# Optimization experiments

Hardware: AMD Instinct MI355X
Metric: run time of the kernel (lower is better)

## Reference

```python
import jax, jax.numpy as jnp
import numpy as np

N_USERS = 100000
N_MOVIES = 100000
N_EDGES = 1000000
HIDDEN = 128


def setup_inputs() -> dict:
    key = jax.random.key(0)
    k1, k2, k3, k4, k5, k6, k7 = jax.random.split(key, 7)
    user_features = jax.random.normal(k1, (N_USERS, HIDDEN), dtype=jnp.float32)
    movie_features = jax.random.normal(k2, (N_MOVIES, HIDDEN), dtype=jnp.float32)
    src = jax.random.randint(k3, (N_EDGES,), 0, N_USERS, dtype=jnp.int64 if jax.config.jax_enable_x64 else jnp.int32)
    dst = jax.random.randint(k4, (N_EDGES,), 0, N_MOVIES, dtype=jnp.int64 if jax.config.jax_enable_x64 else jnp.int32)
    edge_index = jnp.stack([src, dst], axis=0)
    # Linear(2*HIDDEN, HIDDEN) params, torch-style init (kaiming uniform ~ U(-1/sqrt(fan_in), 1/sqrt(fan_in)))
    b1_bound = 1.0 / np.sqrt(2 * HIDDEN)
    W1 = jax.random.uniform(k5, (2 * HIDDEN, HIDDEN), minval=-b1_bound, maxval=b1_bound, dtype=jnp.float32)
    b1 = jax.random.uniform(k6, (HIDDEN,), minval=-b1_bound, maxval=b1_bound, dtype=jnp.float32)
    b2_bound = 1.0 / np.sqrt(HIDDEN)
    k8, k9 = jax.random.split(k7)
    W2 = jax.random.uniform(k8, (HIDDEN, 1), minval=-b2_bound, maxval=b2_bound, dtype=jnp.float32)
    b2 = jax.random.uniform(k9, (1,), minval=-b2_bound, maxval=b2_bound, dtype=jnp.float32)
    return {"user_features": user_features, "movie_features": movie_features,
            "edge_index": edge_index, "W1": W1, "b1": b1, "W2": W2, "b2": b2}


def reference(user_features, movie_features, edge_index, W1, b1, W2, b2):
    # Gather endpoint features per edge: [E, H] each
    u = user_features[edge_index[0]]
    m = movie_features[edge_index[1]]
    edge_feats = jnp.concatenate([u, m], axis=1)  # [E, 2H]
    h = jax.nn.relu(edge_feats @ W1 + b1)         # [E, H]
    out = h @ W2 + b2                             # [E, 1]
    return out.reshape(-1)
```

## Files before the change

### kernel.cpp

```cpp
#include <hip/hip_runtime.h>
#include <hip/hip_bf16.h>

typedef short s8v __attribute__((ext_vector_type(8)));
typedef float f4v __attribute__((ext_vector_type(4)));

__device__ __forceinline__ unsigned int bfround(float f) {
    unsigned int x = __float_as_uint(f);
    return (x + 0x7fffu + ((x >> 16) & 1u)) >> 16;
}
__device__ __forceinline__ unsigned int pkbf(float x, float y) {
    __hip_bfloat162 h = __float22bfloat162_rn(make_float2(x, y));
    return *(unsigned int*)&h;
}
__device__ __forceinline__ float i8f(unsigned int w, int k) {
    return (float)((int)(signed char)(w >> (8 * k)));
}

__global__ __launch_bounds__(256) void pack_w(const float* __restrict__ W1,
                                              uint4* __restrict__ WF)
{
    const int half = blockIdx.x;
    #pragma unroll
    for (int iter = 0; iter < 8; ++iter) {
        int idx  = iter * 256 + threadIdx.x;
        int lane = idx & 63;
        int t    = (idx >> 6) & 7;
        int c    = idx >> 9;
        int q = lane >> 4, m = lane & 15;
        unsigned int w[4];
        #pragma unroll
        for (int jj = 0; jj < 4; ++jj) {
            float lo = W1[(size_t)(half * 128 + c * 32 + q * 8 + 2 * jj    ) * 128 + t * 16 + m];
            float hi = W1[(size_t)(half * 128 + c * 32 + q * 8 + 2 * jj + 1) * 128 + t * 16 + m];
            w[jj] = bfround(lo) | (bfround(hi) << 16);
        }
        WF[(size_t)half * 2048 + idx] = make_uint4(w[0], w[1], w[2], w[3]);
    }
}

__global__ __launch_bounds__(256, 2) void proj_kernel(
    const float* __restrict__ userf, const float* __restrict__ movief,
    const uint4* __restrict__ WF, const float* __restrict__ b1,
    uint2* __restrict__ Pu, uint2* __restrict__ Pm,
    float* __restrict__ SU, float* __restrict__ SM,
    int ntiles, int bph)
{
    const int half = blockIdx.x >= bph;
    const int bid  = half ? blockIdx.x - bph : blockIdx.x;
    const float* __restrict__ feat = half ? movief : userf;
    uint2* __restrict__ P = half ? Pm : Pu;
    float* __restrict__ S = half ? SM : SU;
    const uint4* __restrict__ wfh = WF + (size_t)half * 2048;

    const int lane = threadIdx.x & 63;
    const int m    = lane & 15;
    const int q    = lane >> 4;

    s8v bfrag[8][4];
    #pragma unroll
    for (int c = 0; c < 4; ++c)
        #pragma unroll
        for (int t = 0; t < 8; ++t) {
            uint4 f = wfh[(c * 8 + t) * 64 + lane];
            bfrag[t][c] = *(const s8v*)&f;
        }

    float bias_v[8];
    #pragma unroll
    for (int t = 0; t < 8; ++t)
        bias_v[t] = half ? b1[t * 16 + m] : 0.0f;

    const int wid = bid * 4 + (threadIdx.x >> 6);
    const int nw  = bph * 4;

#define LOAD_A(dst, t_) do {                                            \
        const float4* arow_ = (const float4*)feat + (size_t)(t_) * 512; \
        _Pragma("unroll")                                               \
        for (int c_ = 0; c_ < 4; ++c_) {                                \
            dst[c_][0] = arow_[m * 32 + c_ * 8 + q * 2 + 0];            \
            dst[c_][1] = arow_[m * 32 + c_ * 8 + q * 2 + 1];            \
        }                                                               \
    } while (0)

    float4 a[4][2];
    int tile = wid;
    if (tile < ntiles) LOAD_A(a, tile);

    while (tile < ntiles) {
        const int nxt = tile + nw;
        float4 an[4][2];
        if (nxt < ntiles) LOAD_A(an, nxt);

        f4v acc[8];
        #pragma unroll
        for (int t = 0; t < 8; ++t)
            acc[t] = (f4v){bias_v[t], bias_v[t], bias_v[t], bias_v[t]};

        #pragma unroll
        for (int c = 0; c < 4; ++c) {
            uint4 aw;
            aw.x = pkbf(a[c][0].x, a[c][0].y);
            aw.y = pkbf(a[c][0].z, a[c][0].w);
            aw.z = pkbf(a[c][1].x, a[c][1].y);
            aw.w = pkbf(a[c][1].z, a[c][1].w);
            s8v af = *(const s8v*)&aw;

            #pragma unroll
            for (int t = 0; t < 8; ++t)
                acc[t] = __builtin_amdgcn_mfma_f32_16x16x32_bf16(af, bfrag[t][c], acc[t], 0, 0, 0);
        }

        #pragma unroll
        for (int r = 0; r < 4; ++r) {
            float mx = 0.0f;
            #pragma unroll
            for (int t = 0; t < 8; ++t) mx = fmaxf(mx, fabsf(acc[t][r]));
            #pragma unroll
            for (int off = 1; off < 16; off <<= 1)
                mx = fmaxf(mx, __shfl_xor(mx, off, 64));
            float inv = mx > 0.0f ? 127.0f / mx : 0.0f;

            unsigned int lo = 0, hi = 0;
            #pragma unroll
            for (int t = 0; t < 4; ++t) {
                lo |= ((unsigned int)(__float2int_rn(acc[t][r]     * inv) & 0xff)) << (8 * t);
                hi |= ((unsigned int)(__float2int_rn(acc[t + 4][r] * inv) & 0xff)) << (8 * t);
            }
            int row = tile * 16 + q * 4 + r;
            P[(size_t)row * 16 + m] = make_uint2(lo, hi);
            if (m == 0) S[row] = mx * (1.0f / 127.0f);
        }

        #pragma unroll
        for (int c = 0; c < 4; ++c) {
            a[c][0] = an[c][0];
            a[c][1] = an[c][1];
        }
        tile = nxt;
    }
#undef LOAD_A
}

__global__ __launch_bounds__(256) void edge_kernel(
    const int* __restrict__ src, const int* __restrict__ dst,
    const uint2* __restrict__ Pu, const uint2* __restrict__ Pm,
    const float* __restrict__ SU, const float* __restrict__ SM,
    const float* __restrict__ W2, const float* __restrict__ b2,
    float* __restrict__ out)
{
    const int lane = threadIdx.x & 63;
    const int L    = lane & 15;
    const int g    = lane >> 4;
    const int eg   = (blockIdx.x * 4 + (threadIdx.x >> 6)) * 16 + g * 4;

    float w2v[8];
    #pragma unroll
    for (int j = 0; j < 8; ++j) w2v[j] = W2[j * 16 + L];

    int si[4], di[4];
    #pragma unroll
    for (int i = 0; i < 4; ++i) { si[i] = src[eg + i]; di[i] = dst[eg + i]; }

    uint2 pu[4], pm[4];
    float scu[4], scm[4];
    #pragma unroll
    for (int i = 0; i < 4; ++i) {
        pu[i] = Pu[(size_t)si[i] * 16 + L];
        pm[i] = Pm[(size_t)di[i] * 16 + L];
        scu[i] = SU[si[i]];
        scm[i] = SM[di[i]];
    }

    float res[4];
    #pragma unroll
    for (int i = 0; i < 4; ++i) {
        const unsigned int uw[2] = {pu[i].x, pu[i].y};
        const unsigned int mw[2] = {pm[i].x, pm[i].y};
        float acc = 0.0f;
        #pragma unroll
        for (int v = 0; v < 2; ++v) {
            #pragma unroll
            for (int k = 0; k < 4; ++k) {
                float h = fmaf(scu[i], i8f(uw[v], k), scm[i] * i8f(mw[v], k));
                acc = fmaf(fmaxf(h, 0.0f), w2v[v * 4 + k], acc);
            }
        }
        #pragma unroll
        for (int off = 1; off < 16; off <<= 1)
            acc += __shfl_xor(acc, off, 64);
        res[i] = acc;
    }

    if (L == 0) {
        float bb = b2[0];
        *(float4*)(out + eg) = make_float4(res[0] + bb, res[1] + bb, res[2] + bb, res[3] + bb);
    }
}

extern "C" void kernel_launch(void* const* d_in, const int* in_sizes, int n_in,
                              void* d_out, int out_size, void* d_ws, size_t ws_size,
                              hipStream_t stream) {
    const float* userf  = (const float*)d_in[0];
    const float* movief = (const float*)d_in[1];
    const int*   eidx   = (const int*)d_in[2];
    const float* W1     = (const float*)d_in[3];
    const float* b1     = (const float*)d_in[4];
    const float* W2     = (const float*)d_in[5];
    const float* b2     = (const float*)d_in[6];
    float* out = (float*)d_out;

    const int NU = in_sizes[0] / 128;
    const int NM = in_sizes[1] / 128;
    const int E  = in_sizes[2] / 2;

    uint2* Pu = (uint2*)d_ws;
    uint2* Pm = Pu + (size_t)NU * 16;
    float* SU = (float*)(Pm + (size_t)NM * 16);
    float* SM = SU + NU;
    uint4* WF = (uint4*)(SM + NM);

    const int ntiles = NU / 16;
    const int bph    = 512;

    pack_w<<<2, 256, 0, stream>>>(W1, WF);
    proj_kernel<<<2 * bph, 256, 0, stream>>>(userf, movief, WF, b1, Pu, Pm, SU, SM, ntiles, bph);
    edge_kernel<<<E / 64, 256, 0, stream>>>(eidx, eidx + E, Pu, Pm, SU, SM, W2, b2, out);
}
```

Baseline: 184.9 us.

## Deepen proj_kernel prefetch to two tiles and coalesce scale stores

```diff
diff --git a/kernel.cpp b/kernel.cpp
--- a/kernel.cpp
+++ b/kernel.cpp
@@ -82,14 +82,14 @@
         }                                                               \
     } while (0)
 
-    float4 a[4][2];
+    float4 a0[4][2], a1[4][2], a2[4][2];
     int tile = wid;
-    if (tile < ntiles) LOAD_A(a, tile);
+    if (tile < ntiles)          LOAD_A(a0, tile);
+    if (tile + nw < ntiles)     LOAD_A(a1, tile + nw);
 
     while (tile < ntiles) {
-        const int nxt = tile + nw;
-        float4 an[4][2];
-        if (nxt < ntiles) LOAD_A(an, nxt);
+        const int pf = tile + 2 * nw;
+        if (pf < ntiles) LOAD_A(a2, pf);
 
         f4v acc[8];
         #pragma unroll
@@ -99,10 +99,10 @@
         #pragma unroll
         for (int c = 0; c < 4; ++c) {
             uint4 aw;
-            aw.x = pkbf(a[c][0].x, a[c][0].y);
-            aw.y = pkbf(a[c][0].z, a[c][0].w);
-            aw.z = pkbf(a[c][1].x, a[c][1].y);
-            aw.w = pkbf(a[c][1].z, a[c][1].w);
+            aw.x = pkbf(a0[c][0].x, a0[c][0].y);
+            aw.y = pkbf(a0[c][0].z, a0[c][0].w);
+            aw.z = pkbf(a0[c][1].x, a0[c][1].y);
+            aw.w = pkbf(a0[c][1].z, a0[c][1].w);
             s8v af = *(const s8v*)&aw;
 
             #pragma unroll
@@ -110,6 +110,7 @@
                 acc[t] = __builtin_amdgcn_mfma_f32_16x16x32_bf16(af, bfrag[t][c], acc[t], 0, 0, 0);
         }
 
+        float snv[4];
         #pragma unroll
         for (int r = 0; r < 4; ++r) {
             float mx = 0.0f;
@@ -119,6 +120,7 @@
             for (int off = 1; off < 16; off <<= 1)
                 mx = fmaxf(mx, __shfl_xor(mx, off, 64));
             float inv = mx > 0.0f ? 127.0f / mx : 0.0f;
+            snv[r] = mx * (1.0f / 127.0f);
 
             unsigned int lo = 0, hi = 0;
             #pragma unroll
@@ -128,15 +130,25 @@
             }
             int row = tile * 16 + q * 4 + r;
             P[(size_t)row * 16 + m] = make_uint2(lo, hi);
-            if (m == 0) S[row] = mx * (1.0f / 127.0f);
+        }
+
+        {
+            float t0 = __shfl(snv[0], (lane >> 2 & 3) << 4, 64);
+            float t1 = __shfl(snv[1], (lane >> 2 & 3) << 4, 64);
+            float t2 = __shfl(snv[2], (lane >> 2 & 3) << 4, 64);
+            float t3 = __shfl(snv[3], (lane >> 2 & 3) << 4, 64);
+            float v01 = (lane & 1) ? t1 : t0;
+            float v23 = (lane & 1) ? t3 : t2;
+            float val = (lane & 2) ? v23 : v01;
+            if (lane < 16) S[tile * 16 + lane] = val;
         }
 
         #pragma unroll
         for (int c = 0; c < 4; ++c) {
-            a[c][0] = an[c][0];
-            a[c][1] = an[c][1];
-        }
-        tile = nxt;
+            a0[c][0] = a1[c][0]; a0[c][1] = a1[c][1];
+            a1[c][0] = a2[c][0]; a1[c][1] = a2[c][1];
+        }
+        tile += nw;
     }
 #undef LOAD_A
 }
```

New measurement: 210.3 us. +13.7%, slower.
